# Performance work log

Hardware: AMD Instinct MI355X
Metric: run time of the kernel (lower is better)

The kernel has to match this reference:

```python
import jax, jax.numpy as jnp
import numpy as np

N_GENES, N_CELLS = 10000, 8192
Z_DIM, G_REP_DIM, K_DIM, H_DIM = 100, 100, 32, 256
GB_TAU = 1.0


def setup_inputs() -> dict:
    key = jax.random.key(0)
    ks = jax.random.split(key, 12)
    s = lambda fan_in: 1.0 / np.sqrt(fan_in)
    return {
        "raw_Z": jax.random.normal(ks[0], (Z_DIM, N_CELLS), jnp.float32),
        "gen_Z": jax.random.normal(ks[1], (Z_DIM, N_CELLS), jnp.float32),
        "G_rep": jax.random.normal(ks[2], (N_GENES, G_REP_DIM), jnp.float32)
                 * np.sqrt(2.0 / (N_GENES + G_REP_DIM)),  # xavier_normal
        # pre-sampled Gumbel(0,1) noise for gumbel_softmax
        "gumbel": jax.random.gumbel(ks[3], (N_GENES, N_CELLS), jnp.float32),
        # key_Z MLP: Linear(z_col_dim->h_dim), GELU, Linear(h_dim->k_dim); stored as (in,out)
        "Wz1": jax.random.uniform(ks[4], (Z_DIM, H_DIM), jnp.float32, -s(Z_DIM), s(Z_DIM)),
        "bz1": jax.random.uniform(ks[5], (H_DIM,), jnp.float32, -s(Z_DIM), s(Z_DIM)),
        "Wz2": jax.random.uniform(ks[6], (H_DIM, K_DIM), jnp.float32, -s(H_DIM), s(H_DIM)),
        "bz2": jax.random.uniform(ks[7], (K_DIM,), jnp.float32, -s(H_DIM), s(H_DIM)),
        # key_G MLP: Linear(g_rep_dim->k_dim), GELU, Linear(k_dim->k_dim)
        "Wg1": jax.random.uniform(ks[8], (G_REP_DIM, K_DIM), jnp.float32, -s(G_REP_DIM), s(G_REP_DIM)),
        "bg1": jax.random.uniform(ks[9], (K_DIM,), jnp.float32, -s(G_REP_DIM), s(G_REP_DIM)),
        "Wg2": jax.random.uniform(ks[10], (K_DIM, K_DIM), jnp.float32, -s(K_DIM), s(K_DIM)),
        "bg2": jax.random.uniform(ks[11], (K_DIM,), jnp.float32, -s(K_DIM), s(K_DIM)),
    }


def reference(raw_Z, gen_Z, G_rep, gumbel, Wz1, bz1, Wz2, bz2, Wg1, bg1, Wg2, bg2):
    # key_Z MLP over cells: (n_cells, z_dim) -> (n_cells, k_dim)
    Zc = raw_Z.T
    key = jax.nn.gelu(Zc @ Wz1 + bz1, approximate=False) @ Wz2 + bz2
    # key_G MLP over genes: (n_genes, g_rep_dim) -> (n_genes, k_dim)
    query = jax.nn.gelu(G_rep @ Wg1 + bg1, approximate=False) @ Wg2 + bg2
    d_k = query.shape[-1]
    scores = (query @ key.T) / jnp.sqrt(jnp.asarray(d_k, jnp.float32))  # (n_genes, n_cells)
    # gumbel_softmax(hard=False): softmax((logits + Gumbel noise) / tau)
    p_attn = jax.nn.softmax((scores + gumbel) / GB_TAU, axis=-1)
    X_hat_means = p_attn @ gen_Z.T  # (n_genes, z_dim)
    return X_hat_means.T  # (z_dim, n_genes)
```

## Files before the change

### kernel.cpp

```cpp
#include <hip/hip_runtime.h>
#include <hip/hip_bf16.h>

typedef __attribute__((ext_vector_type(8))) short short8;
typedef __attribute__((ext_vector_type(4))) float f32x4;
typedef __attribute__((ext_vector_type(4))) unsigned uint4v;
typedef __attribute__((ext_vector_type(2))) unsigned uint2v;

#define NCELL 8192
#define NGENE 10000
#define KD 32
#define ZD 100
#define HD 256
#define GD 100
#define NGB 625
#define NGPAD 10016
#define QSL 16

__device__ __forceinline__ float gelu_exact(float x) {
    return 0.5f * x * (1.0f + erff(x * 0.70710678118654752f));
}
__device__ __forceinline__ ushort bf16bits(float x) {
    __hip_bfloat16 h = __float2bfloat16(x);
    return *reinterpret_cast<ushort*>(&h);
}
__device__ __forceinline__ f32x4 ld4(const float* p) {
    return *reinterpret_cast<const f32x4*>(p);
}
__device__ __forceinline__ short8 ld8(const ushort* p) {
    return *reinterpret_cast<const short8*>(p);
}

__global__ void key_kernel(const float* __restrict__ rawZ,
                           const float* __restrict__ Wz1, const float* __restrict__ bz1,
                           const float* __restrict__ Wz2, const float* __restrict__ bz2,
                           ushort* __restrict__ khiA, ushort* __restrict__ kloA,
                           unsigned* __restrict__ kmax2u) {
    __shared__ float z[8][ZD];
    __shared__ float h[8][HD];
    const int t = threadIdx.x;
    const int c0 = blockIdx.x * 8;
    for (int idx = t; idx < 8 * ZD; idx += 256) {
        int cell = idx / ZD, i = idx - cell * ZD;
        z[cell][i] = rawZ[i * NCELL + c0 + cell];
    }
    __syncthreads();
    float a[8];
#pragma unroll
    for (int cl = 0; cl < 8; ++cl) a[cl] = bz1[t];
    for (int i = 0; i < ZD; ++i) {
        float wv = Wz1[i * HD + t];
#pragma unroll
        for (int cl = 0; cl < 8; ++cl) a[cl] += z[cl][i] * wv;
    }
#pragma unroll
    for (int cl = 0; cl < 8; ++cl) h[cl][t] = gelu_exact(a[cl]);
    __syncthreads();
    const int cell = t >> 5, kk = t & 31;
    float b = bz2[kk];
    for (int j = 0; j < HD; ++j) b += h[cell][j] * Wz2[j * KD + kk];
    const int c = c0 + cell;
    const int c16 = c & 15;
    const int G = c16 >> 2;
    const int s = (c16 & 3) | ((((G & 1) << 1) | (G >> 1)) << 2);
    __hip_bfloat16 hi = __float2bfloat16(b);
    float hif = __bfloat162float(hi);
    int idx = ((c >> 4) * 64 + s + 16 * (kk >> 3)) * 8 + (kk & 7);
    khiA[idx] = *reinterpret_cast<ushort*>(&hi);
    kloA[idx] = bf16bits(b - hif);
    float sq = b * b;
#pragma unroll
    for (int off = 16; off > 0; off >>= 1) sq += __shfl_xor(sq, off, 32);
    if (kk == 0) atomicMax(kmax2u, __float_as_uint(sq));
}

__global__ void query_kernel(const float* __restrict__ Grep,
                             const float* __restrict__ Wg1, const float* __restrict__ bg1,
                             const float* __restrict__ Wg2, const float* __restrict__ bg2,
                             const unsigned* __restrict__ kmax2u,
                             ushort* __restrict__ qBhi, ushort* __restrict__ qBlo,
                             float* __restrict__ Mg) {
    __shared__ float gr[8][GD];
    __shared__ float hq[8][KD];
    const int t = threadIdx.x;
    const int g0 = blockIdx.x * 8;
    for (int idx = t; idx < 8 * GD; idx += 256) {
        int ge = idx / GD, i = idx - ge * GD;
        int g = g0 + ge;
        gr[ge][i] = (g < NGENE) ? Grep[(size_t)g * GD + i] : 0.0f;
    }
    __syncthreads();
    const int ge = t >> 5, kk = t & 31;
    float a = bg1[kk];
    for (int i = 0; i < GD; ++i) a += gr[ge][i] * Wg1[i * KD + kk];
    hq[ge][kk] = gelu_exact(a);
    __syncthreads();
    float b = bg2[kk];
#pragma unroll
    for (int j = 0; j < KD; ++j) b += hq[ge][j] * Wg2[j * KD + kk];
    float qv = b * 0.17677669529663687f;
    const int g = g0 + ge;
    __hip_bfloat16 hi = __float2bfloat16(qv);
    float hif = __bfloat162float(hi);
    int idx = ((g >> 4) * 64 + (g & 15) + 16 * (kk >> 3)) * 8 + (kk & 7);
    qBhi[idx] = *reinterpret_cast<ushort*>(&hi);
    qBlo[idx] = bf16bits(qv - hif);
    float sq = qv * qv;
#pragma unroll
    for (int off = 16; off > 0; off >>= 1) sq += __shfl_xor(sq, off, 32);
    if (kk == 0) {
        float km2 = __uint_as_float(*kmax2u);
        Mg[g] = sqrtf(sq * km2) + 25.0f;
    }
}

__global__ void vprep_kernel(const float* __restrict__ genZ, ushort* __restrict__ genZB) {
    int o = blockIdx.x * 256 + threadIdx.x;
    int j = o & 7;
    int tj = (j & 1) | ((j & 2) << 1) | ((j & 4) >> 1);
    int l = (o >> 3) & 63;
    int cb = (o >> 9) & 255;
    int db = o >> 17;
    int c = cb * 32 + ((l >> 4) & 3) * 8 + tj;
    int d = db * 16 + (l & 15);
    float v = (d < GD) ? genZ[(size_t)d * NCELL + c] : 0.0f;
    genZB[o] = bf16bits(v);
}

#define STEP_COMPUTE(kh0_, kh1_, kl0_, kl1_, u0_, u1_)                                      \
    do {                                                                                    \
        short8 v0 = ld8(vp);         short8 v1 = ld8(vp + 8192);                            \
        short8 v2 = ld8(vp + 16384); short8 v3 = ld8(vp + 24576);                           \
        short8 v4 = ld8(vp + 32768); short8 v5 = ld8(vp + 40960);                           \
        short8 v6 = ld8(vp + 49152); vp += 512;                                             \
        f32x4 s0 = __builtin_amdgcn_mfma_f32_16x16x32_bf16(kh0_, qh, z4, 0, 0, 0);          \
        s0 = __builtin_amdgcn_mfma_f32_16x16x32_bf16(kl0_, qh, s0, 0, 0, 0);                \
        s0 = __builtin_amdgcn_mfma_f32_16x16x32_bf16(kh0_, ql, s0, 0, 0, 0);                \
        f32x4 s1 = __builtin_amdgcn_mfma_f32_16x16x32_bf16(kh1_, qh, z4, 0, 0, 0);          \
        s1 = __builtin_amdgcn_mfma_f32_16x16x32_bf16(kl1_, qh, s1, 0, 0, 0);                \
        s1 = __builtin_amdgcn_mfma_f32_16x16x32_bf16(kh1_, ql, s1, 0, 0, 0);                \
        float p0 = __expf(s0.x + u0_.x + negM);                                             \
        float p1 = __expf(s0.y + u0_.y + negM);                                             \
        float p2 = __expf(s0.z + u0_.z + negM);                                             \
        float p3 = __expf(s0.w + u0_.w + negM);                                             \
        float p4 = __expf(s1.x + u1_.x + negM);                                             \
        float p5 = __expf(s1.y + u1_.y + negM);                                             \
        float p6 = __expf(s1.z + u1_.z + negM);                                             \
        float p7 = __expf(s1.w + u1_.w + negM);                                             \
        L += ((p0 + p1) + (p2 + p3)) + ((p4 + p5) + (p6 + p7));                             \
        unsigned w00, w01, w10, w11;                                                        \
        asm("v_cvt_pk_bf16_f32 %0, %1, %2" : "=v"(w00) : "v"(p0), "v"(p1));                 \
        asm("v_cvt_pk_bf16_f32 %0, %1, %2" : "=v"(w01) : "v"(p2), "v"(p3));                 \
        asm("v_cvt_pk_bf16_f32 %0, %1, %2" : "=v"(w10) : "v"(p4), "v"(p5));                 \
        asm("v_cvt_pk_bf16_f32 %0, %1, %2" : "=v"(w11) : "v"(p6), "v"(p7));                 \
        uint2v rA = __builtin_amdgcn_permlane32_swap(w00, w10, false, false);               \
        uint2v rB = __builtin_amdgcn_permlane32_swap(w01, w11, false, false);               \
        uint4v pau = {rA.x, rA.y, rB.x, rB.y};                                              \
        short8 pa = *reinterpret_cast<short8*>(&pau);                                       \
        acc[0] = __builtin_amdgcn_mfma_f32_16x16x32_bf16(pa, v0, acc[0], 0, 0, 0);          \
        acc[1] = __builtin_amdgcn_mfma_f32_16x16x32_bf16(pa, v1, acc[1], 0, 0, 0);          \
        acc[2] = __builtin_amdgcn_mfma_f32_16x16x32_bf16(pa, v2, acc[2], 0, 0, 0);          \
        acc[3] = __builtin_amdgcn_mfma_f32_16x16x32_bf16(pa, v3, acc[3], 0, 0, 0);          \
        acc[4] = __builtin_amdgcn_mfma_f32_16x16x32_bf16(pa, v4, acc[4], 0, 0, 0);          \
        acc[5] = __builtin_amdgcn_mfma_f32_16x16x32_bf16(pa, v5, acc[5], 0, 0, 0);          \
        acc[6] = __builtin_amdgcn_mfma_f32_16x16x32_bf16(pa, v6, acc[6], 0, 0, 0);          \
    } while (0)

__launch_bounds__(512)
__global__ void fused_kernel(const float* __restrict__ gumbel,
                             const ushort* __restrict__ khiA, const ushort* __restrict__ kloA,
                             const ushort* __restrict__ qBhi, const ushort* __restrict__ qBlo,
                             const float* __restrict__ Mg,
                             const ushort* __restrict__ genZB,
                             float* __restrict__ part, float* __restrict__ Lpart) {
    __shared__ __align__(16) ushort vlds[7 * 8192];
    const int t = threadIdx.x, lane = t & 63, w = t >> 6;
    const int b = blockIdx.x;
    const int q = b & 15;
    const int ib = b >> 4;
    {
        f32x4* vdst = reinterpret_cast<f32x4*>(vlds);
        const f32x4* vsrc = reinterpret_cast<const f32x4*>(genZB);
        for (int i = t; i < 7168; i += 512) {
            int db = i >> 10, rem = i & 1023;
            vdst[i] = vsrc[db * 16384 + q * 1024 + rem];
        }
    }
    __syncthreads();

    const int gx = lane & 15, bq = lane >> 4;
    const int cmap4 = (((bq & 1) << 1) | (bq >> 1)) << 2;
    const ushort* kbase  = khiA + q * 16384 + lane * 8;
    const ushort* klbase = kloA + q * 16384 + lane * 8;
    const f32x4 z4 = {0.f, 0.f, 0.f, 0.f};

    for (int u = ib * 8 + w; u < NGB; u += 128) {
        const float negM = -Mg[u * 16 + gx];
        short8 qh = ld8(qBhi + (size_t)u * 512 + lane * 8);
        short8 ql = ld8(qBlo + (size_t)u * 512 + lane * 8);
        const float* gp = gumbel + (size_t)(u * 16 + gx) * NCELL + q * 512 + cmap4;
        const ushort* kp  = kbase;
        const ushort* klp = klbase;
        const ushort* vp  = vlds + lane * 8;
        f32x4 acc[7];
#pragma unroll
        for (int i = 0; i < 7; ++i) acc[i] = z4;
        float L = 0.f;
        short8 khA0 = ld8(kp),   khA1 = ld8(kp + 512);
        short8 klA0 = ld8(klp),  klA1 = ld8(klp + 512);
        f32x4  uA0  = ld4(gp),   uA1  = ld4(gp + 16);
        kp += 1024; klp += 1024; gp += 32;
        for (int it = 0; it < 7; ++it) {
            short8 khB0 = ld8(kp),   khB1 = ld8(kp + 512);
            short8 klB0 = ld8(klp),  klB1 = ld8(klp + 512);
            f32x4  uB0  = ld4(gp),   uB1  = ld4(gp + 16);
            STEP_COMPUTE(khA0, khA1, klA0, klA1, uA0, uA1);
            khA0 = ld8(kp + 1024);  khA1 = ld8(kp + 1536);
            klA0 = ld8(klp + 1024); klA1 = ld8(klp + 1536);
            uA0  = ld4(gp + 32);    uA1  = ld4(gp + 48);
            kp += 2048; klp += 2048; gp += 64;
            STEP_COMPUTE(khB0, khB1, klB0, klB1, uB0, uB1);
        }
        {
            short8 khB0 = ld8(kp),   khB1 = ld8(kp + 512);
            short8 klB0 = ld8(klp),  klB1 = ld8(klp + 512);
            f32x4  uB0  = ld4(gp),   uB1  = ld4(gp + 16);
            STEP_COMPUTE(khA0, khA1, klA0, klA1, uA0, uA1);
            STEP_COMPUTE(khB0, khB1, klB0, klB1, uB0, uB1);
        }
        L += __shfl_xor(L, 16, 64);
        L += __shfl_xor(L, 32, 64);
        const int wv = q * NGB + u;
        if (lane < 16)
            Lpart[(size_t)wv * 16 + lane] = L;
        float* pp = part + (size_t)wv * 7 * 256;
#pragma unroll
        for (int tile = 0; tile < 7; ++tile)
            *reinterpret_cast<f32x4*>(pp + tile * 256 + lane * 4) = acc[tile];
    }
}

__global__ void combine_kernel(const float* __restrict__ part, const float* __restrict__ Lpart,
                               float* __restrict__ out) {
    const int gb = blockIdx.x;
    const int t = threadIdx.x;
    __shared__ float Linv[16];
    if (t < 16) {
        float s = 0.f;
        for (int qq = 0; qq < QSL; ++qq) s += Lpart[(size_t)(qq * NGB + gb) * 16 + t];
        Linv[t] = 1.0f / s;
    }
    __syncthreads();
    if (t < 448) {
        const int tile = t >> 6, lane = t & 63;
        const int d = tile * 16 + (lane & 15);
        f32x4 ssum = {0.f, 0.f, 0.f, 0.f};
        for (int qq = 0; qq < QSL; ++qq)
            ssum += *reinterpret_cast<const f32x4*>(
                part + ((size_t)(qq * NGB + gb) * 7 + tile) * 256 + lane * 4);
        if (d < GD) {
            const int gl0 = 4 * (lane >> 4);
            f32x4 li = {Linv[gl0], Linv[gl0 + 1], Linv[gl0 + 2], Linv[gl0 + 3]};
            f32x4 o = ssum * li;
            *reinterpret_cast<f32x4*>(out + (size_t)d * NGENE + gb * 16 + gl0) = o;
        }
    }
}

extern "C" void kernel_launch(void* const* d_in, const int* in_sizes, int n_in,
                              void* d_out, int out_size, void* d_ws, size_t ws_size,
                              hipStream_t stream) {
    const float* rawZ  = (const float*)d_in[0];
    const float* genZ  = (const float*)d_in[1];
    const float* Grep  = (const float*)d_in[2];
    const float* gumb  = (const float*)d_in[3];
    const float* Wz1   = (const float*)d_in[4];
    const float* bz1   = (const float*)d_in[5];
    const float* Wz2   = (const float*)d_in[6];
    const float* bz2   = (const float*)d_in[7];
    const float* Wg1   = (const float*)d_in[8];
    const float* bg1   = (const float*)d_in[9];
    const float* Wg2   = (const float*)d_in[10];
    const float* bg2   = (const float*)d_in[11];
    float* out = (float*)d_out;

    char* ws = (char*)d_ws;
    ushort*   khiA  = (ushort*)ws;
    ushort*   kloA  = (ushort*)(ws + 524288);
    ushort*   qBhi  = (ushort*)(ws + 1048576);
    ushort*   qBlo  = (ushort*)(ws + 1703936);
    ushort*   genZB = (ushort*)(ws + 2359296);
    float*    MgA   = (float*)(ws + 4456448);
    unsigned* kmax  = (unsigned*)(ws + 4497408);
    const size_t base_off = 4497664;

    float* partA  = (float*)(ws + base_off);
    float* LpartA = partA + (size_t)QSL * NGB * 7 * 256;

    hipMemsetAsync(kmax, 0, 4, stream);
    hipLaunchKernelGGL(key_kernel,   dim3(NCELL / 8), dim3(256), 0, stream,
                       rawZ, Wz1, bz1, Wz2, bz2, khiA, kloA, kmax);
    hipLaunchKernelGGL(query_kernel, dim3(NGPAD / 8), dim3(256), 0, stream,
                       Grep, Wg1, bg1, Wg2, bg2, kmax, qBhi, qBlo, MgA);
    hipLaunchKernelGGL(vprep_kernel, dim3(917504 / 256), dim3(256), 0, stream,
                       genZ, genZB);
    hipLaunchKernelGGL(fused_kernel, dim3(256), dim3(512), 0, stream,
                       gumb, khiA, kloA, qBhi, qBlo, MgA, genZB, partA, LpartA);
    hipLaunchKernelGGL(combine_kernel, dim3(NGB), dim3(512), 0, stream,
                       partA, LpartA, out);
}
```

Baseline: 196.1 us.

## Process two gene blocks per wave to reuse key and V fragments

Each wave now handles a pair of 16-gene blocks, so every key fragment load and LDS V-fragment load feeds two score/PV MFMA chains instead of one. This halves the key global loads and V LDS reads per gene block and gives the scheduler more independent MFMA and exp work to overlap. The cost is roughly doubled accumulator register use, which may reduce occupancy or cause spills. Gene block 625 is padded: its gumbel row index is clamped and the partial buffers are resized to 626 blocks.

Result: slower. 203.6 us (+3.8%).

```diff
diff --git a/kernel.cpp b/kernel.cpp
--- a/kernel.cpp
+++ b/kernel.cpp
@@ -13,6 +13,8 @@
 #define HD 256
 #define GD 100
 #define NGB 625
+#define NGBU 626
+#define NPAIR 313
 #define NGPAD 10016
 #define QSL 16
 
@@ -29,6 +31,7 @@
 __device__ __forceinline__ short8 ld8(const ushort* p) {
     return *reinterpret_cast<const short8*>(p);
 }
+#define MF(a_, b_, c_) __builtin_amdgcn_mfma_f32_16x16x32_bf16(a_, b_, c_, 0, 0, 0)
 
 __global__ void key_kernel(const float* __restrict__ rawZ,
                            const float* __restrict__ Wz1, const float* __restrict__ bz1,
@@ -126,27 +129,25 @@
     genZB[o] = bf16bits(v);
 }
 
-#define STEP_COMPUTE(kh0_, kh1_, kl0_, kl1_, u0_, u1_)                                      \
+#define STEP2(kh0_, kh1_, kl0_, kl1_, x0_, x1_, y0_, y1_)                                   \
     do {                                                                                    \
         short8 v0 = ld8(vp);         short8 v1 = ld8(vp + 8192);                            \
         short8 v2 = ld8(vp + 16384); short8 v3 = ld8(vp + 24576);                           \
         short8 v4 = ld8(vp + 32768); short8 v5 = ld8(vp + 40960);                           \
         short8 v6 = ld8(vp + 49152); vp += 512;                                             \
-        f32x4 s0 = __builtin_amdgcn_mfma_f32_16x16x32_bf16(kh0_, qh, z4, 0, 0, 0);          \
-        s0 = __builtin_amdgcn_mfma_f32_16x16x32_bf16(kl0_, qh, s0, 0, 0, 0);                \
-        s0 = __builtin_amdgcn_mfma_f32_16x16x32_bf16(kh0_, ql, s0, 0, 0, 0);                \
-        f32x4 s1 = __builtin_amdgcn_mfma_f32_16x16x32_bf16(kh1_, qh, z4, 0, 0, 0);          \
-        s1 = __builtin_amdgcn_mfma_f32_16x16x32_bf16(kl1_, qh, s1, 0, 0, 0);                \
-        s1 = __builtin_amdgcn_mfma_f32_16x16x32_bf16(kh1_, ql, s1, 0, 0, 0);                \
-        float p0 = __expf(s0.x + u0_.x + negM);                                             \
-        float p1 = __expf(s0.y + u0_.y + negM);                                             \
-        float p2 = __expf(s0.z + u0_.z + negM);                                             \
-        float p3 = __expf(s0.w + u0_.w + negM);                                             \
-        float p4 = __expf(s1.x + u1_.x + negM);                                             \
-        float p5 = __expf(s1.y + u1_.y + negM);                                             \
-        float p6 = __expf(s1.z + u1_.z + negM);                                             \
-        float p7 = __expf(s1.w + u1_.w + negM);                                             \
-        L += ((p0 + p1) + (p2 + p3)) + ((p4 + p5) + (p6 + p7));                             \
+        f32x4 sx0 = MF(kh0_, qh0, z4); sx0 = MF(kl0_, qh0, sx0); sx0 = MF(kh0_, ql0, sx0);  \
+        f32x4 sx1 = MF(kh1_, qh0, z4); sx1 = MF(kl1_, qh0, sx1); sx1 = MF(kh1_, ql0, sx1);  \
+        f32x4 sy0 = MF(kh0_, qh1, z4); sy0 = MF(kl0_, qh1, sy0); sy0 = MF(kh0_, ql1, sy0);  \
+        f32x4 sy1 = MF(kh1_, qh1, z4); sy1 = MF(kl1_, qh1, sy1); sy1 = MF(kh1_, ql1, sy1);  \
+        float p0 = __expf(sx0.x + x0_.x + negM0);                                           \
+        float p1 = __expf(sx0.y + x0_.y + negM0);                                           \
+        float p2 = __expf(sx0.z + x0_.z + negM0);                                           \
+        float p3 = __expf(sx0.w + x0_.w + negM0);                                           \
+        float p4 = __expf(sx1.x + x1_.x + negM0);                                           \
+        float p5 = __expf(sx1.y + x1_.y + negM0);                                           \
+        float p6 = __expf(sx1.z + x1_.z + negM0);                                           \
+        float p7 = __expf(sx1.w + x1_.w + negM0);                                           \
+        L0 += ((p0 + p1) + (p2 + p3)) + ((p4 + p5) + (p6 + p7));                            \
         unsigned w00, w01, w10, w11;                                                        \
         asm("v_cvt_pk_bf16_f32 %0, %1, %2" : "=v"(w00) : "v"(p0), "v"(p1));                 \
         asm("v_cvt_pk_bf16_f32 %0, %1, %2" : "=v"(w01) : "v"(p2), "v"(p3));                 \
@@ -154,15 +155,33 @@
         asm("v_cvt_pk_bf16_f32 %0, %1, %2" : "=v"(w11) : "v"(p6), "v"(p7));                 \
         uint2v rA = __builtin_amdgcn_permlane32_swap(w00, w10, false, false);               \
         uint2v rB = __builtin_amdgcn_permlane32_swap(w01, w11, false, false);               \
-        uint4v pau = {rA.x, rA.y, rB.x, rB.y};                                              \
-        short8 pa = *reinterpret_cast<short8*>(&pau);                                       \
-        acc[0] = __builtin_amdgcn_mfma_f32_16x16x32_bf16(pa, v0, acc[0], 0, 0, 0);          \
-        acc[1] = __builtin_amdgcn_mfma_f32_16x16x32_bf16(pa, v1, acc[1], 0, 0, 0);          \
-        acc[2] = __builtin_amdgcn_mfma_f32_16x16x32_bf16(pa, v2, acc[2], 0, 0, 0);          \
-        acc[3] = __builtin_amdgcn_mfma_f32_16x16x32_bf16(pa, v3, acc[3], 0, 0, 0);          \
-        acc[4] = __builtin_amdgcn_mfma_f32_16x16x32_bf16(pa, v4, acc[4], 0, 0, 0);          \
-        acc[5] = __builtin_amdgcn_mfma_f32_16x16x32_bf16(pa, v5, acc[5], 0, 0, 0);          \
-        acc[6] = __builtin_amdgcn_mfma_f32_16x16x32_bf16(pa, v6, acc[6], 0, 0, 0);          \
+        uint4v pau0 = {rA.x, rA.y, rB.x, rB.y};                                             \
+        short8 pa0 = *reinterpret_cast<short8*>(&pau0);                                     \
+        float r0 = __expf(sy0.x + y0_.x + negM1);                                           \
+        float r1 = __expf(sy0.y + y0_.y + negM1);                                           \
+        float r2 = __expf(sy0.z + y0_.z + negM1);                                           \
+        float r3 = __expf(sy0.w + y0_.w + negM1);                                           \
+        float r4 = __expf(sy1.x + y1_.x + negM1);                                           \
+        float r5 = __expf(sy1.y + y1_.y + negM1);                                           \
+        float r6 = __expf(sy1.z + y1_.z + negM1);                                           \
+        float r7 = __expf(sy1.w + y1_.w + negM1);                                           \
+        L1 += ((r0 + r1) + (r2 + r3)) + ((r4 + r5) + (r6 + r7));                            \
+        unsigned x00, x01, x10, x11;                                                        \
+        asm("v_cvt_pk_bf16_f32 %0, %1, %2" : "=v"(x00) : "v"(r0), "v"(r1));                 \
+        asm("v_cvt_pk_bf16_f32 %0, %1, %2" : "=v"(x01) : "v"(r2), "v"(r3));                 \
+        asm("v_cvt_pk_bf16_f32 %0, %1, %2" : "=v"(x10) : "v"(r4), "v"(r5));                 \
+        asm("v_cvt_pk_bf16_f32 %0, %1, %2" : "=v"(x11) : "v"(r6), "v"(r7));                 \
+        uint2v rC = __builtin_amdgcn_permlane32_swap(x00, x10, false, false);               \
+        uint2v rD = __builtin_amdgcn_permlane32_swap(x01, x11, false, false);               \
+        uint4v pau1 = {rC.x, rC.y, rD.x, rD.y};                                             \
+        short8 pa1 = *reinterpret_cast<short8*>(&pau1);                                     \
+        acc0[0] = MF(pa0, v0, acc0[0]);  acc1[0] = MF(pa1, v0, acc1[0]);                    \
+        acc0[1] = MF(pa0, v1, acc0[1]);  acc1[1] = MF(pa1, v1, acc1[1]);                    \
+        acc0[2] = MF(pa0, v2, acc0[2]);  acc1[2] = MF(pa1, v2, acc1[2]);                    \
+        acc0[3] = MF(pa0, v3, acc0[3]);  acc1[3] = MF(pa1, v3, acc1[3]);                    \
+        acc0[4] = MF(pa0, v4, acc0[4]);  acc1[4] = MF(pa1, v4, acc1[4]);                    \
+        acc0[5] = MF(pa0, v5, acc0[5]);  acc1[5] = MF(pa1, v5, acc1[5]);                    \
+        acc0[6] = MF(pa0, v6, acc0[6]);  acc1[6] = MF(pa1, v6, acc1[6]);                    \
     } while (0)
 
 __launch_bounds__(512)
@@ -193,49 +212,67 @@
     const ushort* klbase = kloA + q * 16384 + lane * 8;
     const f32x4 z4 = {0.f, 0.f, 0.f, 0.f};
 
-    for (int u = ib * 8 + w; u < NGB; u += 128) {
-        const float negM = -Mg[u * 16 + gx];
-        short8 qh = ld8(qBhi + (size_t)u * 512 + lane * 8);
-        short8 ql = ld8(qBlo + (size_t)u * 512 + lane * 8);
-        const float* gp = gumbel + (size_t)(u * 16 + gx) * NCELL + q * 512 + cmap4;
+    for (int p = ib * 8 + w; p < NPAIR; p += 128) {
+        const int u0 = 2 * p, u1 = 2 * p + 1;
+        const float negM0 = -Mg[u0 * 16 + gx];
+        const float negM1 = -Mg[u1 * 16 + gx];
+        short8 qh0 = ld8(qBhi + (size_t)u0 * 512 + lane * 8);
+        short8 ql0 = ld8(qBlo + (size_t)u0 * 512 + lane * 8);
+        short8 qh1 = ld8(qBhi + (size_t)u1 * 512 + lane * 8);
+        short8 ql1 = ld8(qBlo + (size_t)u1 * 512 + lane * 8);
+        int grow1 = u1 * 16 + gx;
+        if (grow1 > NGENE - 1) grow1 = NGENE - 1;
+        const float* gp0 = gumbel + (size_t)(u0 * 16 + gx) * NCELL + q * 512 + cmap4;
+        const float* gp1 = gumbel + (size_t)grow1 * NCELL + q * 512 + cmap4;
         const ushort* kp  = kbase;
         const ushort* klp = klbase;
         const ushort* vp  = vlds + lane * 8;
-        f32x4 acc[7];
-#pragma unroll
-        for (int i = 0; i < 7; ++i) acc[i] = z4;
-        float L = 0.f;
+        f32x4 acc0[7], acc1[7];
+#pragma unroll
+        for (int i = 0; i < 7; ++i) { acc0[i] = z4; acc1[i] = z4; }
+        float L0 = 0.f, L1 = 0.f;
         short8 khA0 = ld8(kp),   khA1 = ld8(kp + 512);
         short8 klA0 = ld8(klp),  klA1 = ld8(klp + 512);
-        f32x4  uA0  = ld4(gp),   uA1  = ld4(gp + 16);
-        kp += 1024; klp += 1024; gp += 32;
+        f32x4  xA0  = ld4(gp0),  xA1  = ld4(gp0 + 16);
+        f32x4  yA0  = ld4(gp1),  yA1  = ld4(gp1 + 16);
+        kp += 1024; klp += 1024; gp0 += 32; gp1 += 32;
         for (int it = 0; it < 7; ++it) {
             short8 khB0 = ld8(kp),   khB1 = ld8(kp + 512);
             short8 klB0 = ld8(klp),  klB1 = ld8(klp + 512);
-            f32x4  uB0  = ld4(gp),   uB1  = ld4(gp + 16);
-            STEP_COMPUTE(khA0, khA1, klA0, klA1, uA0, uA1);
+            f32x4  xB0  = ld4(gp0),  xB1  = ld4(gp0 + 16);
+            f32x4  yB0  = ld4(gp1),  yB1  = ld4(gp1 + 16);
+            STEP2(khA0, khA1, klA0, klA1, xA0, xA1, yA0, yA1);
             khA0 = ld8(kp + 1024);  khA1 = ld8(kp + 1536);
             klA0 = ld8(klp + 1024); klA1 = ld8(klp + 1536);
-            uA0  = ld4(gp + 32);    uA1  = ld4(gp + 48);
-            kp += 2048; klp += 2048; gp += 64;
-            STEP_COMPUTE(khB0, khB1, klB0, klB1, uB0, uB1);
+            xA0  = ld4(gp0 + 32);   xA1  = ld4(gp0 + 48);
+            yA0  = ld4(gp1 + 32);   yA1  = ld4(gp1 + 48);
+            kp += 2048; klp += 2048; gp0 += 64; gp1 += 64;
+            STEP2(khB0, khB1, klB0, klB1, xB0, xB1, yB0, yB1);
         }
         {
             short8 khB0 = ld8(kp),   khB1 = ld8(kp + 512);
             short8 klB0 = ld8(klp),  klB1 = ld8(klp + 512);
-            f32x4  uB0  = ld4(gp),   uB1  = ld4(gp + 16);
-            STEP_COMPUTE(khA0, khA1, klA0, klA1, uA0, uA1);
-            STEP_COMPUTE(khB0, khB1, klB0, klB1, uB0, uB1);
-        }
-        L += __shfl_xor(L, 16, 64);
-        L += __shfl_xor(L, 32, 64);
-        const int wv = q * NGB + u;
-        if (lane < 16)
-            Lpart[(size_t)wv * 16 + lane] = L;
-        float* pp = part + (size_t)wv * 7 * 256;
-#pragma unroll
-        for (int tile = 0; tile < 7; ++tile)
-            *reinterpret_cast<f32x4*>(pp + tile * 256 + lane * 4) = acc[tile];
+            f32x4  xB0  = ld4(gp0),  xB1  = ld4(gp0 + 16);
+            f32x4  yB0  = ld4(gp1),  yB1  = ld4(gp1 + 16);
+            STEP2(khA0, khA1, klA0, klA1, xA0, xA1, yA0, yA1);
+            STEP2(khB0, khB1, klB0, klB1, xB0, xB1, yB0, yB1);
+        }
+        L0 += __shfl_xor(L0, 16, 64);
+        L0 += __shfl_xor(L0, 32, 64);
+        L1 += __shfl_xor(L1, 16, 64);
+        L1 += __shfl_xor(L1, 32, 64);
+        const int wv0 = q * NGBU + u0, wv1 = q * NGBU + u1;
+        if (lane < 16) {
+            Lpart[(size_t)wv0 * 16 + lane] = L0;
+            Lpart[(size_t)wv1 * 16 + lane] = L1;
+        }
+        float* pp0 = part + (size_t)wv0 * 7 * 256;
+        float* pp1 = part + (size_t)wv1 * 7 * 256;
+#pragma unroll
+        for (int tile = 0; tile < 7; ++tile) {
+            *reinterpret_cast<f32x4*>(pp0 + tile * 256 + lane * 4) = acc0[tile];
+            *reinterpret_cast<f32x4*>(pp1 + tile * 256 + lane * 4) = acc1[tile];
+        }
     }
 }
 
@@ -246,7 +283,7 @@
     __shared__ float Linv[16];
     if (t < 16) {
         float s = 0.f;
-        for (int qq = 0; qq < QSL; ++qq) s += Lpart[(size_t)(qq * NGB + gb) * 16 + t];
+        for (int qq = 0; qq < QSL; ++qq) s += Lpart[(size_t)(qq * NGBU + gb) * 16 + t];
         Linv[t] = 1.0f / s;
     }
     __syncthreads();
@@ -256,7 +293,7 @@
         f32x4 ssum = {0.f, 0.f, 0.f, 0.f};
         for (int qq = 0; qq < QSL; ++qq)
             ssum += *reinterpret_cast<const f32x4*>(
-                part + ((size_t)(qq * NGB + gb) * 7 + tile) * 256 + lane * 4);
+                part + ((size_t)(qq * NGBU + gb) * 7 + tile) * 256 + lane * 4);
         if (d < GD) {
             const int gl0 = 4 * (lane >> 4);
             f32x4 li = {Linv[gl0], Linv[gl0 + 1], Linv[gl0 + 2], Linv[gl0 + 3]};
@@ -294,7 +331,7 @@
     const size_t base_off = 4497664;
 
     float* partA  = (float*)(ws + base_off);
-    float* LpartA = partA + (size_t)QSL * NGB * 7 * 256;
+    float* LpartA = partA + (size_t)QSL * NGBU * 7 * 256;
 
     hipMemsetAsync(kmax, 0, 4, stream);
     hipLaunchKernelGGL(key_kernel,   dim3(NCELL / 8), dim3(256), 0, stream,
```
